# Kernel tuning notes

Measured on AMD Instinct MI355X. Metric: run time of the kernel, lower is better.

Reference implementation:

```python
import jax, jax.numpy as jnp
import numpy as np
import itertools

COS_THRES = 0.5
TEMP = 0.1
EPS = 1e-06
NUM_MODALS = 3


def _cosine_sim(t1, t2, l1, l2, eps=EPS):
    # t1:[B1,D], t2:[B2,D], l1:[B1,1], l2:[B2,1] -> [B1,B2]
    return jnp.matmul(t1, t2.T) / jnp.maximum(jnp.matmul(l1, l2.T), eps)


def _filtered_infonce(m1, m2, cos_thres=COS_THRES, temp=TEMP, eps=EPS):
    # m1, m2: [B, D]
    B = m1.shape[0]
    l1 = jnp.sqrt(jnp.sum(m1 * m1, axis=-1, keepdims=True))
    l2 = jnp.sqrt(jnp.sum(m2 * m2, axis=-1, keepdims=True))
    cross = _cosine_sim(m1, m2, l1, l2, eps) / temp          # [B,B] logits
    s1 = _cosine_sim(m1, m1, l1, l1, eps)
    s2 = _cosine_sim(m2, m2, l2, l2, eps)
    mask = (s1 <= cos_thres) | (s2 <= cos_thres)
    mask = mask | jnp.eye(B, dtype=bool)                      # diagonal always kept
    # masked row-wise cross entropy with label i == diagonal.
    # Excluding masked columns then re-indexing the label (torch loop) is
    # equivalent to a masked softmax over the full row with label on the diag.
    neg_inf = jnp.asarray(-jnp.inf, cross.dtype)
    logits = jnp.where(mask, cross, neg_inf)
    lse = jax.nn.logsumexp(logits, axis=-1)                   # [B]
    loss_i = lse - jnp.diagonal(cross)                        # [B]
    valid = jnp.sum(mask, axis=-1) > 1                        # rows with >1 candidates
    count = jnp.sum(valid)
    total = jnp.sum(jnp.where(valid, loss_i, 0.0))
    return jnp.where(count > 0, total / jnp.maximum(count, 1), 0.0)


def setup_inputs() -> dict:
    key = jax.random.key(0)
    all_features = jax.random.normal(key, (NUM_MODALS, 4096, 1024), dtype=jnp.float32)
    return {"all_features": all_features}


def reference(all_features) -> jnp.ndarray:
    # CMCLoss with main_modal_idx=None: InfoNCE over all modal pairs.
    n_modals = all_features.shape[0]
    error = 0.0
    num_components = 0
    for i, j in itertools.combinations(range(n_modals), 2):
        error = error + _filtered_infonce(all_features[i], all_features[j])
        num_components += 1
    return error / num_components
```

## Files before the change

### kernel.cpp

```cpp
#include <hip/hip_runtime.h>
#include <stdint.h>
#include <math.h>

typedef float fx4 __attribute__((ext_vector_type(4)));
typedef float fx16 __attribute__((ext_vector_type(16)));
typedef int   ix4 __attribute__((ext_vector_type(4)));
typedef int   ix8 __attribute__((ext_vector_type(8)));

#define NB 4096
#define ND 1024
#define CEPS 1e-6f
#define CTHR 0.5f
#define NT8 8


__device__ __forceinline__ void gload16(const void* g, void* l) {
  __builtin_amdgcn_global_load_lds(
      (const __attribute__((address_space(1))) uint32_t*)(uintptr_t)g,
      (__attribute__((address_space(3))) uint32_t*)(uint32_t)(uintptr_t)l,
      16, 0, 0);
}

__device__ __forceinline__ ix8 ldfrag8(const char* p0, const char* p1) {
  const ix4 lo = *(const ix4*)p0;
  const ix4 hi = *(const ix4*)p1;
  ix8 r;
  r[0] = lo[0]; r[1] = lo[1]; r[2] = lo[2]; r[3] = lo[3];
  r[4] = hi[0]; r[5] = hi[1]; r[6] = hi[2]; r[7] = hi[3];
  return r;
}

#define MFMAS(A, B, C) \
  __builtin_amdgcn_mfma_scale_f32_32x32x64_f8f6f4((A), (B), (C), 0, 0, 0, 127, 0, 127)


__global__ __launch_bounds__(256) void cmc_convert(
    const float* __restrict__ in, uint8_t* __restrict__ xf8,
    float* __restrict__ lnorm) {
  const int row = blockIdx.x;
  const int tid = threadIdx.x;
  const fx4 v = *(const fx4*)(in + (size_t)row * ND + tid * 4);
  int pk = __builtin_amdgcn_cvt_pk_fp8_f32(v[0], v[1], 0, false);
  pk = __builtin_amdgcn_cvt_pk_fp8_f32(v[2], v[3], pk, true);
  ((int*)(xf8 + (size_t)row * ND))[tid] = pk;
  float ss = v[0]*v[0] + v[1]*v[1] + v[2]*v[2] + v[3]*v[3];
  #pragma unroll
  for (int d = 1; d < 64; d <<= 1) ss += __shfl_xor(ss, d);
  __shared__ float sred[4];
  if ((tid & 63) == 0) sred[tid >> 6] = ss;
  __syncthreads();
  if (tid == 0) lnorm[row] = sqrtf(sred[0] + sred[1] + sred[2] + sred[3]);
}


__device__ __forceinline__ void gram128S(
    const uint8_t* __restrict__ Xi, const uint8_t* __restrict__ Xj,
    int rb, int cb, char* smem, int tid, fx16 (&acc)[2][2]) {
  const int l = tid & 63, w = tid >> 6;
  const int wr = w >> 1, wc = w & 1;
  const int srow = tid >> 3;
  const int scol = (((tid & 7) ^ ((tid >> 3) & 7)) << 4);
  const uint8_t* gA = Xi + (size_t)(rb + srow) * ND + scol;
  const uint8_t* gB = Xj + (size_t)(cb + srow) * ND + scol;
  char* dA = smem + tid * 16;
  char* dB = smem + 16384 + tid * 16;

  const int swz = (l & 7) << 4;
  const int kb = (l >> 5) * 32;
  const char* rdA = smem + (wr * 64 + (l & 31)) * 128;
  const char* rdB = smem + 16384 + (wc * 64 + (l & 31)) * 128;

  #pragma unroll
  for (int m = 0; m < 2; ++m)
    #pragma unroll
    for (int n = 0; n < 2; ++n)
      #pragma unroll
      for (int e = 0; e < 16; ++e) acc[m][n][e] = 0.f;

  #pragma unroll 1
  for (int t = 0; t < NT8; ++t) {
    const int k0 = t * 128;
    #pragma unroll
    for (int s = 0; s < 4; ++s) {
      gload16(gA + (size_t)s * 32 * ND + k0, dA + s * 4096);
      gload16(gB + (size_t)s * 32 * ND + k0, dB + s * 4096);
    }
    __syncthreads();
    #pragma unroll
    for (int ks = 0; ks < 2; ++ks) {
      const int c0 = (ks * 64 + kb) ^ swz;
      const int c1 = (ks * 64 + kb + 16) ^ swz;
      ix8 A[2], B[2];
      A[0] = ldfrag8(rdA + c0,        rdA + c1);
      A[1] = ldfrag8(rdA + 4096 + c0, rdA + 4096 + c1);
      B[0] = ldfrag8(rdB + c0,        rdB + c1);
      B[1] = ldfrag8(rdB + 4096 + c0, rdB + 4096 + c1);
      acc[0][0] = MFMAS(A[0], B[0], acc[0][0]);
      acc[0][1] = MFMAS(A[0], B[1], acc[0][1]);
      acc[1][0] = MFMAS(A[1], B[0], acc[1][0]);
      acc[1][1] = MFMAS(A[1], B[1], acc[1][1]);
    }
    __syncthreads();
  }
}


__global__ __launch_bounds__(256, 4) void cmc_selfmask(
    const uint8_t* __restrict__ xf8, const float* __restrict__ lnorm,
    uint32_t* __restrict__ maskw) {
  __shared__ __align__(16) char smem[32768];
  const int o = blockIdx.x;
  const int bid = (o & 7) * 198 + (o >> 3);
  const int md = bid / 528;
  int k = bid - md * 528;
  int by = 0;
  while (k >= 32 - by) { k -= 32 - by; ++by; }
  const int bx = by + k;
  const int rb = by * 128, cb = bx * 128;
  const int tid = threadIdx.x;
  const int l = tid & 63, w = tid >> 6;
  const int wr = w >> 1, wc = w & 1;

  const uint8_t* X = xf8 + (size_t)md * NB * ND;
  fx16 acc[2][2];
  gram128S(X, X, rb, cb, smem, tid, acc);

  uint32_t* tile = (uint32_t*)smem;
  float* Lr = (float*)(smem + 2048);
  float* Lc = (float*)(smem + 2560);
  if (tid < 128) {
    Lr[tid] = lnorm[md * NB + rb + tid];
    Lc[tid] = lnorm[md * NB + cb + tid];
  }
  __syncthreads();

  #pragma unroll
  for (int m = 0; m < 2; ++m)
    #pragma unroll
    for (int r = 0; r < 16; ++r) {
      const int rl0 = wr * 64 + m * 32 + (r & 3) + 8 * (r >> 2);
      const float Lrv = Lr[rl0 + 4 * (l >> 5)];
      #pragma unroll
      for (int n = 0; n < 2; ++n) {
        const int cl = wc * 64 + n * 32 + (l & 31);
        const float cv = acc[m][n][r] / fmaxf(Lrv * Lc[cl], CEPS);
        const uint64_t b = __ballot(cv <= CTHR);
        if (l == 0)  tile[(rl0 + 0) * 4 + wc * 2 + n] = (uint32_t)b;
        if (l == 32) tile[(rl0 + 4) * 4 + wc * 2 + n] = (uint32_t)(b >> 32);
      }
    }
  __syncthreads();

  for (int t = tid; t < 512; t += 256) {
    const int row = t >> 2, wd = t & 3;
    maskw[((size_t)md * NB + rb + row) * 128 + (cb >> 5) + wd] = tile[t];
  }
  if (by != bx) {
    for (int t = tid; t < 512; t += 256) {
      const int crow = t & 127;
      const int wp = t >> 7;
      uint32_t wv = 0;
      #pragma unroll
      for (int r = 0; r < 32; ++r) {
        const uint32_t bit = (tile[(wp * 32 + r) * 4 + (crow >> 5)] >> (crow & 31)) & 1u;
        wv |= bit << r;
      }
      maskw[((size_t)md * NB + cb + crow) * 128 + (rb >> 5) + wp] = wv;
    }
  }
}


__global__ __launch_bounds__(256, 4) void cmc_pair(
    const uint8_t* __restrict__ xf8, const float* __restrict__ lnorm,
    const uint32_t* __restrict__ maskw,
    float* __restrict__ sumexp, float* __restrict__ cntrow,
    float* __restrict__ diagv) {
  __shared__ __align__(16) char smem[32768];
  const int o = blockIdx.x;
  const int bid = (o & 7) * 384 + (o >> 3);
  const int p = bid >> 10;
  const int rem = bid & 1023;
  const int by = rem >> 5, bx = rem & 31;
  const int mi = (p == 2) ? 1 : 0;
  const int mj = (p == 0) ? 1 : 2;
  const int rb = by * 128, cb = bx * 128;
  const int tid = threadIdx.x;
  const int l = tid & 63, w = tid >> 6;
  const int wr = w >> 1, wc = w & 1;

  const uint8_t* Xi = xf8 + (size_t)mi * NB * ND;
  const uint8_t* Xj = xf8 + (size_t)mj * NB * ND;

  fx16 acc[2][2];
  gram128S(Xi, Xj, rb, cb, smem, tid, acc);

  uint32_t* Mt = (uint32_t*)smem;
  float* Lri = (float*)(smem + 4096);
  float* Lcj = (float*)(smem + 4608);
  for (int t = tid; t < 512; t += 256) {
    const int row = t >> 2, wd = t & 3;
    Mt[t]       = maskw[((size_t)mi * NB + rb + row) * 128 + (cb >> 5) + wd];
    Mt[512 + t] = maskw[((size_t)mj * NB + rb + row) * 128 + (cb >> 5) + wd];
  }
  if (tid < 128) {
    Lri[tid] = lnorm[mi * NB + rb + tid];
    Lcj[tid] = lnorm[mj * NB + cb + tid];
  }
  __syncthreads();

  #pragma unroll
  for (int m = 0; m < 2; ++m)
    #pragma unroll
    for (int r = 0; r < 16; ++r) {
      const int rl = wr * 64 + m * 32 + (r & 3) + 8 * (r >> 2) + 4 * (l >> 5);
      const int rg = rb + rl;
      const float Lrv = Lri[rl];
      float se = 0.f, ct = 0.f;
      #pragma unroll
      for (int n = 0; n < 2; ++n) {
        const int cl = wc * 64 + n * 32 + (l & 31);
        const int cg = cb + cl;
        const uint32_t bi = (Mt[rl * 4 + (cl >> 5)] >> (cl & 31)) & 1u;
        const uint32_t bj = (Mt[512 + rl * 4 + (cl >> 5)] >> (cl & 31)) & 1u;
        const bool msk = bi | bj | (rg == cg);
        const float logit = acc[m][n][r] / fmaxf(Lrv * Lcj[cl], CEPS) * 10.0f;
        if (rg == cg) diagv[p * NB + rg] = logit;
        if (msk) { se += __expf(logit); ct += 1.f; }
      }
      #pragma unroll
      for (int d = 1; d < 32; d <<= 1) {
        se += __shfl_xor(se, d);
        ct += __shfl_xor(ct, d);
      }
      if ((l & 31) == 0) {
        atomicAdd(&sumexp[p * NB + rg], se);
        atomicAdd(&cntrow[p * NB + rg], ct);
      }
    }
}


__global__ __launch_bounds__(256) void cmc_final(
    const float* __restrict__ sumexp, const float* __restrict__ cntrow,
    const float* __restrict__ diagv, float* __restrict__ out) {
  const int tid = threadIdx.x;
  __shared__ float sred[8];
  float lsum = 0.f;
  for (int p = 0; p < 3; ++p) {
    float t = 0.f, c = 0.f;
    for (int r = tid; r < NB; r += 256) {
      const float cnt = cntrow[p * NB + r];
      if (cnt > 1.0f) {
        t += logf(sumexp[p * NB + r]) - diagv[p * NB + r];
        c += 1.f;
      }
    }
    #pragma unroll
    for (int d = 1; d < 64; d <<= 1) { t += __shfl_xor(t, d); c += __shfl_xor(c, d); }
    if ((tid & 63) == 0) { sred[(tid >> 6) * 2] = t; sred[(tid >> 6) * 2 + 1] = c; }
    __syncthreads();
    if (tid == 0) {
      const float tt = sred[0] + sred[2] + sred[4] + sred[6];
      const float cc = sred[1] + sred[3] + sred[5] + sred[7];
      lsum += (cc > 0.f) ? tt / fmaxf(cc, 1.f) : 0.f;
    }
    __syncthreads();
  }
  if (tid == 0) out[0] = lsum / 3.0f;
}


extern "C" void kernel_launch(void* const* d_in, const int* in_sizes, int n_in,
                              void* d_out, int out_size, void* d_ws, size_t ws_size,
                              hipStream_t stream) {
  const float* in = (const float*)d_in[0];
  float* out = (float*)d_out;
  char* ws = (char*)d_ws;

  const size_t X8_BYTES = (size_t)3 * NB * ND;
  uint8_t* xf8  = (uint8_t*)ws;
  float* lnorm  = (float*)(ws + X8_BYTES);
  float* sumexp = lnorm + 3 * NB;
  float* cntrow = sumexp + 3 * NB;
  float* diagv  = cntrow + 3 * NB;
  uint32_t* maskw = (uint32_t*)(diagv + 3 * NB);

  hipMemsetAsync(sumexp, 0, (size_t)2 * 3 * NB * sizeof(float), stream);

  cmc_convert<<<3 * NB, 256, 0, stream>>>(in, xf8, lnorm);
  cmc_selfmask<<<1584, 256, 0, stream>>>(xf8, lnorm, maskw);
  cmc_pair<<<3072, 256, 0, stream>>>(xf8, lnorm, maskw, sumexp, cntrow, diagv);
  cmc_final<<<1, 256, 0, stream>>>(sumexp, cntrow, diagv, out);
}
```

Baseline: 213.8 us.

## Enlarge Gram tiles to 256x256 with 512-thread blocks and shallower K steps

Both Gram kernels (self-mask and cross-pair) now compute 256x256 output tiles with 8 waves per block instead of 128x128 tiles with 4 waves. Each wave computes 2x4 MFMA blocks per K step, and each K step stages 64 bytes of K instead of 128. This doubles operand reuse per byte loaded from global memory and cuts the block count. The risks are a halved grid (768/408 blocks), twice as many barrier-synchronized iterations, a narrower 4-way LDS swizzle that may cause bank conflicts, and more accumulator registers per thread.

After: 266.8 us. 24.8% more time.

```diff
diff --git a/kernel.cpp b/kernel.cpp
--- a/kernel.cpp
+++ b/kernel.cpp
@@ -11,7 +11,7 @@
 #define ND 1024
 #define CEPS 1e-6f
 #define CTHR 0.5f
-#define NT8 8
+#define NT16 16
 
 
 __device__ __forceinline__ void gload16(const void* g, void* l) {
@@ -53,82 +53,80 @@
 }
 
 
-__device__ __forceinline__ void gram128S(
+__device__ __forceinline__ void gram256S(
     const uint8_t* __restrict__ Xi, const uint8_t* __restrict__ Xj,
-    int rb, int cb, char* smem, int tid, fx16 (&acc)[2][2]) {
+    int rb, int cb, char* smem, int tid, fx16 (&acc)[2][4]) {
   const int l = tid & 63, w = tid >> 6;
   const int wr = w >> 1, wc = w & 1;
-  const int srow = tid >> 3;
-  const int scol = (((tid & 7) ^ ((tid >> 3) & 7)) << 4);
+  const int srow = tid >> 2;
+  const int scol = (((tid & 3) ^ (srow & 3)) << 4);
   const uint8_t* gA = Xi + (size_t)(rb + srow) * ND + scol;
   const uint8_t* gB = Xj + (size_t)(cb + srow) * ND + scol;
   char* dA = smem + tid * 16;
   char* dB = smem + 16384 + tid * 16;
 
-  const int swz = (l & 7) << 4;
+  const int swz = (l & 3) << 4;
   const int kb = (l >> 5) * 32;
-  const char* rdA = smem + (wr * 64 + (l & 31)) * 128;
-  const char* rdB = smem + 16384 + (wc * 64 + (l & 31)) * 128;
+  const char* rdA = smem + (wr * 64 + (l & 31)) * 64;
+  const char* rdB = smem + 16384 + (wc * 128 + (l & 31)) * 64;
 
   #pragma unroll
   for (int m = 0; m < 2; ++m)
     #pragma unroll
-    for (int n = 0; n < 2; ++n)
+    for (int n = 0; n < 4; ++n)
       #pragma unroll
       for (int e = 0; e < 16; ++e) acc[m][n][e] = 0.f;
 
   #pragma unroll 1
-  for (int t = 0; t < NT8; ++t) {
-    const int k0 = t * 128;
-    #pragma unroll
-    for (int s = 0; s < 4; ++s) {
-      gload16(gA + (size_t)s * 32 * ND + k0, dA + s * 4096);
-      gload16(gB + (size_t)s * 32 * ND + k0, dB + s * 4096);
-    }
-    __syncthreads();
-    #pragma unroll
-    for (int ks = 0; ks < 2; ++ks) {
-      const int c0 = (ks * 64 + kb) ^ swz;
-      const int c1 = (ks * 64 + kb + 16) ^ swz;
-      ix8 A[2], B[2];
-      A[0] = ldfrag8(rdA + c0,        rdA + c1);
-      A[1] = ldfrag8(rdA + 4096 + c0, rdA + 4096 + c1);
-      B[0] = ldfrag8(rdB + c0,        rdB + c1);
-      B[1] = ldfrag8(rdB + 4096 + c0, rdB + 4096 + c1);
-      acc[0][0] = MFMAS(A[0], B[0], acc[0][0]);
-      acc[0][1] = MFMAS(A[0], B[1], acc[0][1]);
-      acc[1][0] = MFMAS(A[1], B[0], acc[1][0]);
-      acc[1][1] = MFMAS(A[1], B[1], acc[1][1]);
-    }
-    __syncthreads();
-  }
-}
-
-
-__global__ __launch_bounds__(256, 4) void cmc_selfmask(
+  for (int t = 0; t < NT16; ++t) {
+    const int k0 = t * 64;
+    gload16(gA + k0, dA);
+    gload16(gA + (size_t)128 * ND + k0, dA + 8192);
+    gload16(gB + k0, dB);
+    gload16(gB + (size_t)128 * ND + k0, dB + 8192);
+    __syncthreads();
+    const int c0 = kb ^ swz;
+    const int c1 = (kb + 16) ^ swz;
+    ix8 A[2], B[4];
+    A[0] = ldfrag8(rdA + c0,        rdA + c1);
+    A[1] = ldfrag8(rdA + 2048 + c0, rdA + 2048 + c1);
+    #pragma unroll
+    for (int n = 0; n < 4; ++n)
+      B[n] = ldfrag8(rdB + n * 2048 + c0, rdB + n * 2048 + c1);
+    #pragma unroll
+    for (int m = 0; m < 2; ++m)
+      #pragma unroll
+      for (int n = 0; n < 4; ++n)
+        acc[m][n] = MFMAS(A[m], B[n], acc[m][n]);
+    __syncthreads();
+  }
+}
+
+
+__global__ __launch_bounds__(512, 2) void cmc_selfmask(
     const uint8_t* __restrict__ xf8, const float* __restrict__ lnorm,
     uint32_t* __restrict__ maskw) {
   __shared__ __align__(16) char smem[32768];
   const int o = blockIdx.x;
-  const int bid = (o & 7) * 198 + (o >> 3);
-  const int md = bid / 528;
-  int k = bid - md * 528;
+  const int bid = (o & 7) * 51 + (o >> 3);
+  const int md = bid / 136;
+  int k = bid - md * 136;
   int by = 0;
-  while (k >= 32 - by) { k -= 32 - by; ++by; }
+  while (k >= 16 - by) { k -= 16 - by; ++by; }
   const int bx = by + k;
-  const int rb = by * 128, cb = bx * 128;
+  const int rb = by * 256, cb = bx * 256;
   const int tid = threadIdx.x;
   const int l = tid & 63, w = tid >> 6;
   const int wr = w >> 1, wc = w & 1;
 
   const uint8_t* X = xf8 + (size_t)md * NB * ND;
-  fx16 acc[2][2];
-  gram128S(X, X, rb, cb, smem, tid, acc);
+  fx16 acc[2][4];
+  gram256S(X, X, rb, cb, smem, tid, acc);
 
   uint32_t* tile = (uint32_t*)smem;
-  float* Lr = (float*)(smem + 2048);
-  float* Lc = (float*)(smem + 2560);
-  if (tid < 128) {
+  float* Lr = (float*)(smem + 8192);
+  float* Lc = (float*)(smem + 9216);
+  if (tid < 256) {
     Lr[tid] = lnorm[md * NB + rb + tid];
     Lc[tid] = lnorm[md * NB + cb + tid];
   }
@@ -141,28 +139,28 @@
       const int rl0 = wr * 64 + m * 32 + (r & 3) + 8 * (r >> 2);
       const float Lrv = Lr[rl0 + 4 * (l >> 5)];
       #pragma unroll
-      for (int n = 0; n < 2; ++n) {
-        const int cl = wc * 64 + n * 32 + (l & 31);
+      for (int n = 0; n < 4; ++n) {
+        const int cl = wc * 128 + n * 32 + (l & 31);
         const float cv = acc[m][n][r] / fmaxf(Lrv * Lc[cl], CEPS);
         const uint64_t b = __ballot(cv <= CTHR);
-        if (l == 0)  tile[(rl0 + 0) * 4 + wc * 2 + n] = (uint32_t)b;
-        if (l == 32) tile[(rl0 + 4) * 4 + wc * 2 + n] = (uint32_t)(b >> 32);
-      }
-    }
-  __syncthreads();
-
-  for (int t = tid; t < 512; t += 256) {
-    const int row = t >> 2, wd = t & 3;
+        if (l == 0)  tile[(rl0 + 0) * 8 + wc * 4 + n] = (uint32_t)b;
+        if (l == 32) tile[(rl0 + 4) * 8 + wc * 4 + n] = (uint32_t)(b >> 32);
+      }
+    }
+  __syncthreads();
+
+  for (int t = tid; t < 2048; t += 512) {
+    const int row = t >> 3, wd = t & 7;
     maskw[((size_t)md * NB + rb + row) * 128 + (cb >> 5) + wd] = tile[t];
   }
   if (by != bx) {
-    for (int t = tid; t < 512; t += 256) {
-      const int crow = t & 127;
-      const int wp = t >> 7;
+    for (int t = tid; t < 2048; t += 512) {
+      const int crow = t & 255;
+      const int wp = t >> 8;
       uint32_t wv = 0;
       #pragma unroll
       for (int r = 0; r < 32; ++r) {
-        const uint32_t bit = (tile[(wp * 32 + r) * 4 + (crow >> 5)] >> (crow & 31)) & 1u;
+        const uint32_t bit = (tile[(wp * 32 + r) * 8 + (crow >> 5)] >> (crow & 31)) & 1u;
         wv |= bit << r;
       }
       maskw[((size_t)md * NB + cb + crow) * 128 + (rb >> 5) + wp] = wv;
@@ -171,20 +169,20 @@
 }
 
 
-__global__ __launch_bounds__(256, 4) void cmc_pair(
+__global__ __launch_bounds__(512, 2) void cmc_pair(
     const uint8_t* __restrict__ xf8, const float* __restrict__ lnorm,
     const uint32_t* __restrict__ maskw,
     float* __restrict__ sumexp, float* __restrict__ cntrow,
     float* __restrict__ diagv) {
   __shared__ __align__(16) char smem[32768];
   const int o = blockIdx.x;
-  const int bid = (o & 7) * 384 + (o >> 3);
-  const int p = bid >> 10;
-  const int rem = bid & 1023;
-  const int by = rem >> 5, bx = rem & 31;
+  const int bid = (o & 7) * 96 + (o >> 3);
+  const int p = bid >> 8;
+  const int rem = bid & 255;
+  const int by = rem >> 4, bx = rem & 15;
   const int mi = (p == 2) ? 1 : 0;
   const int mj = (p == 0) ? 1 : 2;
-  const int rb = by * 128, cb = bx * 128;
+  const int rb = by * 256, cb = bx * 256;
   const int tid = threadIdx.x;
   const int l = tid & 63, w = tid >> 6;
   const int wr = w >> 1, wc = w & 1;
@@ -192,18 +190,18 @@
   const uint8_t* Xi = xf8 + (size_t)mi * NB * ND;
   const uint8_t* Xj = xf8 + (size_t)mj * NB * ND;
 
-  fx16 acc[2][2];
-  gram128S(Xi, Xj, rb, cb, smem, tid, acc);
+  fx16 acc[2][4];
+  gram256S(Xi, Xj, rb, cb, smem, tid, acc);
 
   uint32_t* Mt = (uint32_t*)smem;
-  float* Lri = (float*)(smem + 4096);
-  float* Lcj = (float*)(smem + 4608);
-  for (int t = tid; t < 512; t += 256) {
-    const int row = t >> 2, wd = t & 3;
-    Mt[t]       = maskw[((size_t)mi * NB + rb + row) * 128 + (cb >> 5) + wd];
-    Mt[512 + t] = maskw[((size_t)mj * NB + rb + row) * 128 + (cb >> 5) + wd];
-  }
-  if (tid < 128) {
+  float* Lri = (float*)(smem + 16384);
+  float* Lcj = (float*)(smem + 17408);
+  for (int t = tid; t < 2048; t += 512) {
+    const int row = t >> 3, wd = t & 7;
+    Mt[t]        = maskw[((size_t)mi * NB + rb + row) * 128 + (cb >> 5) + wd];
+    Mt[2048 + t] = maskw[((size_t)mj * NB + rb + row) * 128 + (cb >> 5) + wd];
+  }
+  if (tid < 256) {
     Lri[tid] = lnorm[mi * NB + rb + tid];
     Lcj[tid] = lnorm[mj * NB + cb + tid];
   }
@@ -218,11 +216,11 @@
       const float Lrv = Lri[rl];
       float se = 0.f, ct = 0.f;
       #pragma unroll
-      for (int n = 0; n < 2; ++n) {
-        const int cl = wc * 64 + n * 32 + (l & 31);
+      for (int n = 0; n < 4; ++n) {
+        const int cl = wc * 128 + n * 32 + (l & 31);
         const int cg = cb + cl;
-        const uint32_t bi = (Mt[rl * 4 + (cl >> 5)] >> (cl & 31)) & 1u;
-        const uint32_t bj = (Mt[512 + rl * 4 + (cl >> 5)] >> (cl & 31)) & 1u;
+        const uint32_t bi = (Mt[rl * 8 + (cl >> 5)] >> (cl & 31)) & 1u;
+        const uint32_t bj = (Mt[2048 + rl * 8 + (cl >> 5)] >> (cl & 31)) & 1u;
         const bool msk = bi | bj | (rg == cg);
         const float logit = acc[m][n][r] / fmaxf(Lrv * Lcj[cl], CEPS) * 10.0f;
         if (rg == cg) diagv[p * NB + rg] = logit;
@@ -289,7 +287,7 @@
   hipMemsetAsync(sumexp, 0, (size_t)2 * 3 * NB * sizeof(float), stream);
 
   cmc_convert<<<3 * NB, 256, 0, stream>>>(in, xf8, lnorm);
-  cmc_selfmask<<<1584, 256, 0, stream>>>(xf8, lnorm, maskw);
-  cmc_pair<<<3072, 256, 0, stream>>>(xf8, lnorm, maskw, sumexp, cntrow, diagv);
+  cmc_selfmask<<<408, 512, 0, stream>>>(xf8, lnorm, maskw);
+  cmc_pair<<<768, 512, 0, stream>>>(xf8, lnorm, maskw, sumexp, cntrow, diagv);
   cmc_final<<<1, 256, 0, stream>>>(sumexp, cntrow, diagv, out);
 }
```
